# Performance work log

Measured on AMD Instinct MI355X. Metric: run time of the kernel, lower is better.

The kernel has to match this reference:

```python
import jax, jax.numpy as jnp
import numpy as np

HIDDEN = 2048
KEY_DIM = 2048
NUM_HEADS = 16
EPS = 1e-05


def rms_norm(x, w, eps=EPS):
    ms = jnp.mean(x * x, axis=-1, keepdims=True)
    return x * jax.lax.rsqrt(ms + eps) * w


def setup_inputs() -> dict:
    key = jax.random.key(0)
    ks = jax.random.split(key, 6)
    bound = 1.0 / np.sqrt(HIDDEN)  # kaiming-uniform-ish scale
    x = jax.random.normal(ks[0], (2, 2048, HIDDEN), dtype=jnp.float32)
    rms_w = jnp.ones((HIDDEN,), dtype=jnp.float32)
    Wq = jax.random.uniform(ks[1], (HIDDEN, KEY_DIM), jnp.float32, -bound, bound)
    Wk = jax.random.uniform(ks[2], (HIDDEN, KEY_DIM), jnp.float32, -bound, bound)
    Wv = jax.random.uniform(ks[3], (HIDDEN, KEY_DIM), jnp.float32, -bound, bound)
    Wo = jax.random.uniform(ks[4], (KEY_DIM, HIDDEN), jnp.float32, -bound, bound)
    return {"x": x, "rms_w": rms_w, "Wq": Wq, "Wk": Wk, "Wv": Wv, "Wo": Wo}


def reference(x, rms_w, Wq, Wk, Wv, Wo):
    B, S, _ = x.shape
    residual = x
    xn = rms_norm(x, rms_w)
    # project and split heads: [B,S,H,Dh]
    q = (xn @ Wq).reshape(B, S, NUM_HEADS, KEY_DIM // NUM_HEADS)
    k = (xn @ Wk).reshape(B, S, NUM_HEADS, KEY_DIM // NUM_HEADS)
    v = (xn @ Wv).reshape(B, S, NUM_HEADS, KEY_DIM // NUM_HEADS)
    # NOTE: original scales by 1/sqrt(key_dim), not head_dim — kept faithful
    scale = 1.0 / jnp.sqrt(jnp.float32(KEY_DIM))
    scores = jnp.einsum('bshd,bthd->bhst', q, k) * scale  # [B,H,S,S]
    causal = jnp.tril(jnp.ones((S, S), dtype=bool))
    scores = jnp.where(causal[None, None], scores, -jnp.inf)
    probs = jax.nn.softmax(scores, axis=-1)  # stable max-subtract internally
    out = jnp.einsum('bhst,bthd->bshd', probs, v).reshape(B, S, KEY_DIM)
    return out @ Wo + residual
```

## Files before the change

kernel.cpp:

```cpp
#include <hip/hip_runtime.h>
#include <math.h>

typedef __attribute__((ext_vector_type(8))) short bf16x8;
typedef __attribute__((ext_vector_type(4))) float f32x4;
typedef __attribute__((ext_vector_type(16))) float f32x16;

#define HID 2048
#define SEQ 2048
#define NH  16
#define DH  128
#define QS_LOG2E 0.0318793607f

__device__ __forceinline__ ushort f2bf(float f) {
  union { float f; unsigned u; } v; v.f = f;
  unsigned r = v.u + 0x7fffu + ((v.u >> 16) & 1u);
  return (ushort)(r >> 16);
}

__device__ __forceinline__ void gload16(const ushort* g, ushort* l) {
  __builtin_amdgcn_global_load_lds((const __attribute__((address_space(1))) void*)g,
                                   (__attribute__((address_space(3))) void*)l,
                                   16, 0, 0);
}

__global__ __launch_bounds__(256) void k_transpose4(const float* __restrict__ W0,
                                                    const float* __restrict__ W1,
                                                    const float* __restrict__ W2,
                                                    const float* __restrict__ W3,
                                                    ushort* __restrict__ T0,
                                                    ushort* __restrict__ T3) {
  __shared__ float t[32][33];
  int z = blockIdx.z;
  const float* W = (z == 0) ? W0 : (z == 1) ? W1 : (z == 2) ? W2 : W3;
  ushort* Wt = (z == 3) ? T3 : (T0 + (size_t)z * 2048 * 2048);
  int n0 = blockIdx.x * 32, k0 = blockIdx.y * 32;
  int tx = threadIdx.x, ty = threadIdx.y;
  for (int i = ty; i < 32; i += 8)
    t[i][tx] = W[(size_t)(k0 + i) * HID + n0 + tx];
  __syncthreads();
  for (int i = ty; i < 32; i += 8)
    Wt[(size_t)(n0 + i) * HID + k0 + tx] = f2bf(t[tx][i]);
}

__global__ __launch_bounds__(256) void k_rmsnorm(const float* __restrict__ x,
                                                 const float* __restrict__ w,
                                                 ushort* __restrict__ xn) {
  int row = blockIdx.x;
  const float* xr = x + (size_t)row * HID;
  int base = threadIdx.x * 8;
  float4 a = *(const float4*)(xr + base);
  float4 c = *(const float4*)(xr + base + 4);
  float ss = a.x*a.x + a.y*a.y + a.z*a.z + a.w*a.w
           + c.x*c.x + c.y*c.y + c.z*c.z + c.w*c.w;
  #pragma unroll
  for (int off = 32; off > 0; off >>= 1) ss += __shfl_xor(ss, off);
  __shared__ float red[4];
  if ((threadIdx.x & 63) == 0) red[threadIdx.x >> 6] = ss;
  __syncthreads();
  float tot = red[0] + red[1] + red[2] + red[3];
  float sc = rsqrtf(tot * (1.0f / HID) + 1e-5f);
  float4 wa = *(const float4*)(w + base);
  float4 wc = *(const float4*)(w + base + 4);
  ushort h[8];
  h[0] = f2bf(a.x * sc * wa.x); h[1] = f2bf(a.y * sc * wa.y);
  h[2] = f2bf(a.z * sc * wa.z); h[3] = f2bf(a.w * sc * wa.w);
  h[4] = f2bf(c.x * sc * wc.x); h[5] = f2bf(c.y * sc * wc.y);
  h[6] = f2bf(c.z * sc * wc.z); h[7] = f2bf(c.w * sc * wc.w);
  int4 pk;
  pk.x = h[0] | ((int)h[1] << 16);
  pk.y = h[2] | ((int)h[3] << 16);
  pk.z = h[4] | ((int)h[5] << 16);
  pk.w = h[6] | ((int)h[7] << 16);
  *(int4*)&xn[(size_t)row * HID + base] = pk;
}

__global__ __launch_bounds__(256) void k_gemm9(const ushort* __restrict__ A,
                                               const ushort* __restrict__ Bt,
                                               ushort* __restrict__ obf,
                                               ushort* __restrict__ vt) {
  constexpr int K = 2048;
  __shared__ ushort sA[128 * 64];
  __shared__ ushort sB[128 * 64];
  const int tid = threadIdx.x;
  const int lane = tid & 63, w = tid >> 6;
  const int wr = w >> 1, wc = w & 1;
  const int bm = blockIdx.y, bn = blockIdx.x;
  const int g = lane >> 4, l15 = lane & 15;
  f32x4 acc[4][4];
  #pragma unroll
  for (int i = 0; i < 4; ++i)
    #pragma unroll
    for (int j = 0; j < 4; ++j) acc[i][j] = f32x4{0.f, 0.f, 0.f, 0.f};

  const ushort* ap[4];
  const ushort* bp[4];
  ushort* la[4];
  ushort* lb[4];
  #pragma unroll
  for (int c = 0; c < 4; ++c) {
    int id = (w * 4 + c) * 64 + lane;
    int r = id >> 3, ck = id & 7;
    int ke = (ck ^ (r & 7)) * 8;
    ap[c] = &A[(size_t)(bm * 128 + r) * K + ke];
    bp[c] = &Bt[(size_t)(bn * 128 + r) * K + ke];
    la[c] = ((ushort*)sA) + (w * 4 + c) * 512;
    lb[c] = ((ushort*)sB) + (w * 4 + c) * 512;
  }

  const int nt = K / 64;
  #pragma unroll 1
  for (int t = 0; t < nt; ++t) {
    #pragma unroll
    for (int c = 0; c < 4; ++c) {
      gload16(ap[c], la[c]);
      gload16(bp[c], lb[c]);
      ap[c] += 64;
      bp[c] += 64;
    }
    __syncthreads();
    #pragma unroll
    for (int kk = 0; kk < 2; ++kk) {
      bf16x8 aF[4], bF[4];
      #pragma unroll
      for (int i = 0; i < 4; ++i) {
        int row = wr * 64 + i * 16 + l15;
        int cp = (kk * 4 + g) ^ (lane & 7);
        aF[i] = *(const bf16x8*)&sA[row * 64 + cp * 8];
      }
      #pragma unroll
      for (int j = 0; j < 4; ++j) {
        int row = wc * 64 + j * 16 + l15;
        int cp = (kk * 4 + g) ^ (lane & 7);
        bF[j] = *(const bf16x8*)&sB[row * 64 + cp * 8];
      }
      #pragma unroll
      for (int i = 0; i < 4; ++i)
        #pragma unroll
        for (int j = 0; j < 4; ++j)
          acc[i][j] = __builtin_amdgcn_mfma_f32_16x16x32_bf16(aF[i], bF[j], acc[i][j], 0, 0, 0);
    }
    __syncthreads();
  }

  int rbase = bm * 128 + wr * 64 + g * 4;
  int cbase = bn * 128 + wc * 64 + l15;
  if (bn < 32) {
    const float sc = (bn < 16) ? QS_LOG2E : 1.0f;
    #pragma unroll
    for (int i = 0; i < 4; ++i) {
      #pragma unroll
      for (int j = 0; j < 4; ++j) {
        int col = cbase + j * 16;
        #pragma unroll
        for (int r = 0; r < 4; ++r) {
          int row = rbase + i * 16 + r;
          obf[(size_t)row * 4096 + col] = f2bf(acc[i][j][r] * sc);
        }
      }
    }
  } else {
    #pragma unroll
    for (int i = 0; i < 4; ++i) {
      int rowb = rbase + i * 16;
      int b = rowb >> 11, s = rowb & 2047;
      #pragma unroll
      for (int j = 0; j < 4; ++j) {
        int nv = cbase + j * 16 - 4096;
        int h = nv >> 7, d = nv & 127;
        uint lo = (uint)f2bf(acc[i][j][0]) | ((uint)f2bf(acc[i][j][1]) << 16);
        uint hi = (uint)f2bf(acc[i][j][2]) | ((uint)f2bf(acc[i][j][3]) << 16);
        uint2 pk = {lo, hi};
        *(uint2*)&vt[(size_t)((b * NH + h) * DH + d) * SEQ + s] = pk;
      }
    }
  }
}

__global__ __launch_bounds__(256) void k_gemm7o(const ushort* __restrict__ A,
                                                const ushort* __restrict__ Bt,
                                                float* __restrict__ ofl,
                                                const float* __restrict__ resid,
                                                int K) {
  __shared__ ushort sA[128 * 64];
  __shared__ ushort sB[128 * 64];
  const int tid = threadIdx.x;
  const int lane = tid & 63, w = tid >> 6;
  const int wr = w >> 1, wc = w & 1;
  const int bm = blockIdx.y, bn = blockIdx.x;
  const int g = lane >> 4, l15 = lane & 15;
  f32x4 acc[4][4];
  #pragma unroll
  for (int i = 0; i < 4; ++i)
    #pragma unroll
    for (int j = 0; j < 4; ++j) acc[i][j] = f32x4{0.f, 0.f, 0.f, 0.f};

  const ushort* ap[4];
  const ushort* bp[4];
  ushort* la[4];
  ushort* lb[4];
  #pragma unroll
  for (int c = 0; c < 4; ++c) {
    int id = (w * 4 + c) * 64 + lane;
    int r = id >> 3, ck = id & 7;
    int ke = (ck ^ (r & 7)) * 8;
    ap[c] = &A[(size_t)(bm * 128 + r) * K + ke];
    bp[c] = &Bt[(size_t)(bn * 128 + r) * K + ke];
    la[c] = ((ushort*)sA) + (w * 4 + c) * 512;
    lb[c] = ((ushort*)sB) + (w * 4 + c) * 512;
  }

  const int nt = K / 64;
  #pragma unroll 1
  for (int t = 0; t < nt; ++t) {
    #pragma unroll
    for (int c = 0; c < 4; ++c) {
      gload16(ap[c], la[c]);
      gload16(bp[c], lb[c]);
      ap[c] += 64;
      bp[c] += 64;
    }
    __syncthreads();
    #pragma unroll
    for (int kk = 0; kk < 2; ++kk) {
      bf16x8 aF[4], bF[4];
      #pragma unroll
      for (int i = 0; i < 4; ++i) {
        int row = wr * 64 + i * 16 + l15;
        int cp = (kk * 4 + g) ^ (lane & 7);
        aF[i] = *(const bf16x8*)&sA[row * 64 + cp * 8];
      }
      #pragma unroll
      for (int j = 0; j < 4; ++j) {
        int row = wc * 64 + j * 16 + l15;
        int cp = (kk * 4 + g) ^ (lane & 7);
        bF[j] = *(const bf16x8*)&sB[row * 64 + cp * 8];
      }
      #pragma unroll
      for (int i = 0; i < 4; ++i)
        #pragma unroll
        for (int j = 0; j < 4; ++j)
          acc[i][j] = __builtin_amdgcn_mfma_f32_16x16x32_bf16(aF[i], bF[j], acc[i][j], 0, 0, 0);
    }
    __syncthreads();
  }

  int rbase = bm * 128 + wr * 64 + g * 4;
  int cbase = bn * 128 + wc * 64 + l15;
  #pragma unroll
  for (int i = 0; i < 4; ++i) {
    #pragma unroll
    for (int j = 0; j < 4; ++j) {
      int col = cbase + j * 16;
      #pragma unroll
      for (int r = 0; r < 4; ++r) {
        int row = rbase + i * 16 + r;
        ofl[(size_t)row * HID + col] = acc[i][j][r] + resid[(size_t)row * HID + col];
      }
    }
  }
}

__global__ __launch_bounds__(256, 2) void k_attn5(const ushort* __restrict__ qk,
                                                  const ushort* __restrict__ vt,
                                                  ushort* __restrict__ aout) {
  __shared__ ushort sK[64 * 128];
  __shared__ ushort sV[128 * 64];
  const int tid = threadIdx.x;
  const int lane = tid & 63, w = tid >> 6;
  const int h2 = lane >> 5;
  const int l31 = lane & 31;
  const int bid = blockIdx.x;
  const int t = bid >> 3;
  const int u = t & 31, v = t >> 5;
  const int bh = (bid & 7) + 8 * (u & 3);
  const int qblk = v ? 15 - (u >> 2) : (u >> 2);
  const int b = bh >> 4, hh = bh & 15;
  const int q0w = qblk * 128 + w * 32;

  bf16x8 qf[8];
  {
    const ushort* qbase = qk + (size_t)(b * SEQ + q0w + l31) * 4096 + hh * DH;
    #pragma unroll
    for (int kk = 0; kk < 8; ++kk) qf[kk] = *(const bf16x8*)&qbase[kk * 16 + h2 * 8];
  }

  const ushort* kp[4];
  const ushort* vp[4];
  ushort* lk[4];
  ushort* lv[4];
  #pragma unroll
  for (int c = 0; c < 4; ++c) {
    int id = (w * 4 + c) * 64 + lane;
    int kr = id >> 4, ck = id & 15;
    kp[c] = qk + (size_t)(b * SEQ + kr) * 4096 + 2048 + hh * DH + ((ck ^ (kr & 7)) * 8);
    int dr = id >> 3, cv = id & 7;
    vp[c] = vt + (size_t)(bh * DH + dr) * SEQ + ((cv ^ (dr & 7)) * 8);
    lk[c] = ((ushort*)sK) + (size_t)(w * 4 + c) * 512;
    lv[c] = ((ushort*)sV) + (size_t)(w * 4 + c) * 512;
  }

  f32x16 accO[4];
  #pragma unroll
  for (int i = 0; i < 4; ++i)
    #pragma unroll
    for (int r = 0; r < 16; ++r) accO[i][r] = 0.f;
  float l_r = 0.f;

  const int ntile = 2 * qblk + 2;
  #pragma unroll 1
  for (int tt = 0; tt < ntile; ++tt) {
    const int t0 = tt * 64;
    #pragma unroll
    for (int c = 0; c < 4; ++c) {
      gload16(kp[c], lk[c]);
      gload16(vp[c], lv[c]);
      kp[c] += 64 * 4096;
      vp[c] += 64;
    }
    __syncthreads();

    if (t0 <= q0w + 31) {
      f32x16 accS[2];
      #pragma unroll
      for (int i = 0; i < 2; ++i)
        #pragma unroll
        for (int r = 0; r < 16; ++r) accS[i][r] = 0.f;
      #pragma unroll
      for (int kt = 0; kt < 2; ++kt) {
        const int row = kt * 32 + l31;
        #pragma unroll
        for (int kk = 0; kk < 8; ++kk) {
          const int cp = (kk * 2 + h2) ^ (lane & 7);
          bf16x8 kf = *(const bf16x8*)&sK[row * 128 + cp * 8];
          accS[kt] = __builtin_amdgcn_mfma_f32_32x32x16_bf16(kf, qf[kk], accS[kt], 0, 0, 0);
        }
      }
      float rs = 0.f;
      if (t0 + 63 <= q0w) {
        #pragma unroll
        for (int kt = 0; kt < 2; ++kt)
          #pragma unroll
          for (int r = 0; r < 16; ++r) {
            float p = __builtin_amdgcn_exp2f(accS[kt][r]);
            rs += p;
            accS[kt][r] = p;
          }
      } else {
        const int qa = q0w + l31;
        #pragma unroll
        for (int kt = 0; kt < 2; ++kt)
          #pragma unroll
          for (int r = 0; r < 16; ++r) {
            int ka = t0 + kt * 32 + (r & 3) + 8 * (r >> 2) + 4 * h2;
            float p = (ka <= qa) ? __builtin_amdgcn_exp2f(accS[kt][r]) : 0.f;
            rs += p;
            accS[kt][r] = p;
          }
      }
      rs += __shfl_xor(rs, 32);
      l_r += rs;

      uint W[2][4][2];
      #pragma unroll
      for (int kt = 0; kt < 2; ++kt)
        #pragma unroll
        for (int bq = 0; bq < 4; ++bq)
          #pragma unroll
          for (int w2 = 0; w2 < 2; ++w2) {
            uint u0 = __float_as_uint(accS[kt][bq * 4 + w2 * 2]);
            uint u1 = __float_as_uint(accS[kt][bq * 4 + w2 * 2 + 1]);
            W[kt][bq][w2] = (u0 >> 16) | (u1 & 0xffff0000u);
          }
      #pragma unroll
      for (int kc = 0; kc < 4; ++kc) {
        const int kt = kc >> 1, pq = kc & 1;
        uint X0 = W[kt][2 * pq][0],     X1 = W[kt][2 * pq][1];
        uint Y0 = W[kt][2 * pq + 1][0], Y1 = W[kt][2 * pq + 1][1];
        uint sx0 = (uint)__shfl_xor((int)X0, 32);
        uint sx1 = (uint)__shfl_xor((int)X1, 32);
        uint sy0 = (uint)__shfl_xor((int)Y0, 32);
        uint sy1 = (uint)__shfl_xor((int)Y1, 32);
        union { uint u[4]; bf16x8 v; } pu;
        pu.u[0] = h2 ? sy0 : X0;
        pu.u[1] = h2 ? sy1 : X1;
        pu.u[2] = h2 ? Y0 : sx0;
        pu.u[3] = h2 ? Y1 : sx1;
        #pragma unroll
        for (int ds = 0; ds < 4; ++ds) {
          const int dr = ds * 32 + l31;
          const int cp = (kc * 2 + h2) ^ (lane & 7);
          bf16x8 vf = *(const bf16x8*)&sV[dr * 64 + cp * 8];
          accO[ds] = __builtin_amdgcn_mfma_f32_32x32x16_bf16(pu.v, vf, accO[ds], 0, 0, 0);
        }
      }
    }
    __syncthreads();
  }

  float linv = 1.f / l_r;
  #pragma unroll
  for (int r = 0; r < 16; ++r) {
    int qrel = (r & 3) + 8 * (r >> 2) + 4 * h2;
    float li = __shfl(linv, qrel);
    #pragma unroll
    for (int ds = 0; ds < 4; ++ds) {
      aout[(size_t)(b * SEQ + q0w + qrel) * HID + hh * DH + ds * 32 + l31] =
          f2bf(accO[ds][r] * li);
    }
  }
}

extern "C" void kernel_launch(void* const* d_in, const int* in_sizes, int n_in,
                              void* d_out, int out_size, void* d_ws, size_t ws_size,
                              hipStream_t stream) {
  const float* x     = (const float*)d_in[0];
  const float* rms_w = (const float*)d_in[1];
  const float* Wq    = (const float*)d_in[2];
  const float* Wk    = (const float*)d_in[3];
  const float* Wv    = (const float*)d_in[4];
  const float* Wo    = (const float*)d_in[5];
  float* out = (float*)d_out;

  char* ws = (char*)d_ws;
  ushort* WqkvT = (ushort*)ws; ws += (size_t)6144 * 2048 * 2;
  ushort* WoT   = (ushort*)ws; ws += (size_t)2048 * 2048 * 2;
  ushort* xn    = (ushort*)ws; ws += (size_t)4096 * 2048 * 2;
  ushort* qkbuf = (ushort*)ws; ws += (size_t)4096 * 4096 * 2;
  ushort* vt    = (ushort*)ws; ws += (size_t)4096 * 2048 * 2;
  ushort* aout  = (ushort*)ws; ws += (size_t)4096 * 2048 * 2;

  k_transpose4<<<dim3(64, 64, 4), dim3(32, 8), 0, stream>>>(Wq, Wk, Wv, Wo, WqkvT, WoT);

  k_rmsnorm<<<4096, 256, 0, stream>>>(x, rms_w, xn);

  k_gemm9<<<dim3(48, 32), 256, 0, stream>>>(xn, WqkvT, qkbuf, vt);

  k_attn5<<<512, 256, 0, stream>>>(qkbuf, vt, aout);

  k_gemm7o<<<dim3(16, 32), 256, 0, stream>>>(aout, WoT, out, x, 2048);
}
```

Before: 262.6 us.

## Rewrite QKV GEMM with 256x256 tiles, 8 waves, and multi-stage async LDS pipeline

Replaces the 128x128, 4-wave QKV projection GEMM with a 256x256 tile, 512-thread kernel. It uses a double-buffered, half-K-split LDS pipeline: global-to-LDS loads for later stages are issued while MFMAs run on the current stage, with explicit vmcnt waits and raw barriers replacing the __syncthreads pairs. MFMA sections raise wave priority. This aims for more data reuse per LDS byte and to hide memory latency behind compute. The cost is higher register pressure (32 accumulators per wave) and fewer blocks (384) on the GPU.

```diff
diff --git a/kernel.cpp b/kernel.cpp
--- a/kernel.cpp
+++ b/kernel.cpp
@@ -22,6 +22,9 @@
                                    (__attribute__((address_space(3))) void*)l,
                                    16, 0, 0);
 }
+
+#define VMCNT(n) asm volatile("s_waitcnt vmcnt(" #n ")" ::: "memory")
+#define ABAR()   asm volatile("s_barrier" ::: "memory")
 
 __global__ __launch_bounds__(256) void k_transpose4(const float* __restrict__ W0,
                                                     const float* __restrict__ W1,
@@ -74,80 +77,97 @@
   *(int4*)&xn[(size_t)row * HID + base] = pk;
 }
 
-__global__ __launch_bounds__(256) void k_gemm9(const ushort* __restrict__ A,
-                                               const ushort* __restrict__ Bt,
-                                               ushort* __restrict__ obf,
-                                               ushort* __restrict__ vt) {
+__global__ __launch_bounds__(512, 2) void k_gemm10(const ushort* __restrict__ A,
+                                                   const ushort* __restrict__ Bt,
+                                                   ushort* __restrict__ obf,
+                                                   ushort* __restrict__ vt) {
   constexpr int K = 2048;
-  __shared__ ushort sA[128 * 64];
-  __shared__ ushort sB[128 * 64];
+  __shared__ ushort lds[8][8192];
   const int tid = threadIdx.x;
   const int lane = tid & 63, w = tid >> 6;
-  const int wr = w >> 1, wc = w & 1;
+  const int wm = w >> 2, wn = w & 3;
+  const int g = lane >> 4, l15 = lane & 15;
   const int bm = blockIdx.y, bn = blockIdx.x;
-  const int g = lane >> 4, l15 = lane & 15;
-  f32x4 acc[4][4];
-  #pragma unroll
-  for (int i = 0; i < 4; ++i)
+
+  f32x4 acc[8][4];
+  #pragma unroll
+  for (int i = 0; i < 8; ++i)
     #pragma unroll
     for (int j = 0; j < 4; ++j) acc[i][j] = f32x4{0.f, 0.f, 0.f, 0.f};
 
-  const ushort* ap[4];
-  const ushort* bp[4];
-  ushort* la[4];
-  ushort* lb[4];
-  #pragma unroll
-  for (int c = 0; c < 4; ++c) {
-    int id = (w * 4 + c) * 64 + lane;
-    int r = id >> 3, ck = id & 7;
-    int ke = (ck ^ (r & 7)) * 8;
-    ap[c] = &A[(size_t)(bm * 128 + r) * K + ke];
-    bp[c] = &Bt[(size_t)(bn * 128 + r) * K + ke];
-    la[c] = ((ushort*)sA) + (w * 4 + c) * 512;
-    lb[c] = ((ushort*)sB) + (w * 4 + c) * 512;
-  }
-
-  const int nt = K / 64;
+  const ushort* pA[2][2];
+  const ushort* pB[2][2];
+  #pragma unroll
+  for (int kh = 0; kh < 2; ++kh)
+    #pragma unroll
+    for (int L = 0; L < 2; ++L) {
+      int row = L * 128 + w * 16 + (lane >> 2);
+      int ck = (lane & 3) ^ ((row >> 1) & 3);
+      pA[kh][L] = &A[(size_t)(bm * 256 + row) * K + kh * 32 + ck * 8];
+      pB[kh][L] = &Bt[(size_t)(bn * 256 + row) * K + kh * 32 + ck * 8];
+    }
+
+  auto STAGE = [&](int buf, int kh) {
+    ushort* ra = lds[buf * 4 + kh * 2 + 0];
+    ushort* rb = lds[buf * 4 + kh * 2 + 1];
+    #pragma unroll
+    for (int L = 0; L < 2; ++L) {
+      gload16(pA[kh][L], ra + (L * 8 + w) * 512);
+      pA[kh][L] += 64;
+    }
+    #pragma unroll
+    for (int L = 0; L < 2; ++L) {
+      gload16(pB[kh][L], rb + (L * 8 + w) * 512);
+      pB[kh][L] += 64;
+    }
+  };
+
+  auto COMP = [&](int buf, int kh) {
+    const ushort* ra = lds[buf * 4 + kh * 2 + 0];
+    const ushort* rb = lds[buf * 4 + kh * 2 + 1];
+    bf16x8 aF[8], bF[4];
+    #pragma unroll
+    for (int i = 0; i < 8; ++i) {
+      int row = wm * 128 + i * 16 + l15;
+      aF[i] = *(const bf16x8*)&ra[row * 32 + ((g ^ ((row >> 1) & 3)) * 8)];
+    }
+    #pragma unroll
+    for (int j = 0; j < 4; ++j) {
+      int row = wn * 64 + j * 16 + l15;
+      bF[j] = *(const bf16x8*)&rb[row * 32 + ((g ^ ((row >> 1) & 3)) * 8)];
+    }
+    __builtin_amdgcn_s_setprio(1);
+    #pragma unroll
+    for (int i = 0; i < 8; ++i)
+      #pragma unroll
+      for (int j = 0; j < 4; ++j)
+        acc[i][j] = __builtin_amdgcn_mfma_f32_16x16x32_bf16(aF[i], bF[j], acc[i][j], 0, 0, 0);
+    __builtin_amdgcn_s_setprio(0);
+  };
+
+  STAGE(0, 0); STAGE(0, 1); STAGE(1, 0);
+
   #pragma unroll 1
-  for (int t = 0; t < nt; ++t) {
-    #pragma unroll
-    for (int c = 0; c < 4; ++c) {
-      gload16(ap[c], la[c]);
-      gload16(bp[c], lb[c]);
-      ap[c] += 64;
-      bp[c] += 64;
-    }
-    __syncthreads();
-    #pragma unroll
-    for (int kk = 0; kk < 2; ++kk) {
-      bf16x8 aF[4], bF[4];
-      #pragma unroll
-      for (int i = 0; i < 4; ++i) {
-        int row = wr * 64 + i * 16 + l15;
-        int cp = (kk * 4 + g) ^ (lane & 7);
-        aF[i] = *(const bf16x8*)&sA[row * 64 + cp * 8];
-      }
-      #pragma unroll
-      for (int j = 0; j < 4; ++j) {
-        int row = wc * 64 + j * 16 + l15;
-        int cp = (kk * 4 + g) ^ (lane & 7);
-        bF[j] = *(const bf16x8*)&sB[row * 64 + cp * 8];
-      }
-      #pragma unroll
-      for (int i = 0; i < 4; ++i)
-        #pragma unroll
-        for (int j = 0; j < 4; ++j)
-          acc[i][j] = __builtin_amdgcn_mfma_f32_16x16x32_bf16(aF[i], bF[j], acc[i][j], 0, 0, 0);
-    }
-    __syncthreads();
-  }
-
-  int rbase = bm * 128 + wr * 64 + g * 4;
-  int cbase = bn * 128 + wc * 64 + l15;
-  if (bn < 32) {
-    const float sc = (bn < 16) ? QS_LOG2E : 1.0f;
-    #pragma unroll
-    for (int i = 0; i < 4; ++i) {
+  for (int t = 0; t < 30; ++t) {
+    const int b = t & 1, nb = b ^ 1;
+    VMCNT(8); ABAR();
+    STAGE(nb, 1);
+    COMP(b, 0);
+    VMCNT(8); ABAR();
+    STAGE(b, 0);
+    COMP(b, 1);
+  }
+  VMCNT(8); ABAR(); STAGE(1, 1); COMP(0, 0);
+  VMCNT(8); ABAR();               COMP(0, 1);
+  VMCNT(4); ABAR(); COMP(1, 0);
+  VMCNT(0); ABAR(); COMP(1, 1);
+
+  int rbase = bm * 256 + wm * 128 + g * 4;
+  int cbase = bn * 256 + wn * 64 + l15;
+  if (bn < 16) {
+    const float sc = (bn < 8) ? QS_LOG2E : 1.0f;
+    #pragma unroll
+    for (int i = 0; i < 8; ++i) {
       #pragma unroll
       for (int j = 0; j < 4; ++j) {
         int col = cbase + j * 16;
@@ -160,7 +180,7 @@
     }
   } else {
     #pragma unroll
-    for (int i = 0; i < 4; ++i) {
+    for (int i = 0; i < 8; ++i) {
       int rowb = rbase + i * 16;
       int b = rowb >> 11, s = rowb & 2047;
       #pragma unroll
@@ -433,7 +453,7 @@
 
   k_rmsnorm<<<4096, 256, 0, stream>>>(x, rms_w, xn);
 
-  k_gemm9<<<dim3(48, 32), 256, 0, stream>>>(xn, WqkvT, qkbuf, vt);
+  k_gemm10<<<dim3(24, 16), 512, 0, stream>>>(xn, WqkvT, qkbuf, vt);
 
   k_attn5<<<512, 256, 0, stream>>>(qkbuf, vt, aout);
 
```

After: 260.3 us. No clear change (-0.9%).
